# Kernel tuning notes

Hardware: AMD Instinct MI355X
Metric: run time of the kernel (lower is better)

The kernel has to match this reference:

```python
import jax, jax.numpy as jnp
import numpy as np

# real spherical-harmonics constants (3DGS convention)
C0 = 0.28209479177387814
C1 = 0.4886025119029199
C2 = (1.0925484305920792, -1.0925484305920792, 0.31539156525252005, -1.0925484305920792, 0.5462742152960396)
C3 = (-0.5900435899266435, 2.890611442640554, -0.4570457994644658, 0.3731763325901154, -0.4570457994644658, 1.445305721320277, -0.5900435899266435)


def eval_sh3(sh, dirs):
    # sh: [N,16,3], dirs: [N,3] unit view dirs -> [N,3]
    x, y, z = dirs[:, 0:1], dirs[:, 1:2], dirs[:, 2:3]
    xx, yy, zz = x * x, y * y, z * z
    xy, yz, xz = x * y, y * z, x * z
    res = C0 * sh[:, 0]
    res = res - C1 * y * sh[:, 1] + C1 * z * sh[:, 2] - C1 * x * sh[:, 3]
    res = (res + C2[0] * xy * sh[:, 4] + C2[1] * yz * sh[:, 5]
           + C2[2] * (2.0 * zz - xx - yy) * sh[:, 6]
           + C2[3] * xz * sh[:, 7] + C2[4] * (xx - yy) * sh[:, 8])
    res = (res + C3[0] * y * (3.0 * xx - yy) * sh[:, 9] + C3[1] * xy * z * sh[:, 10]
           + C3[2] * y * (4.0 * zz - xx - yy) * sh[:, 11]
           + C3[3] * z * (2.0 * zz - 3.0 * xx - 3.0 * yy) * sh[:, 12]
           + C3[4] * x * (4.0 * zz - xx - yy) * sh[:, 13]
           + C3[5] * z * (xx - yy) * sh[:, 14] + C3[6] * x * (xx - 3.0 * yy) * sh[:, 15])
    return res


def quat_to_rotmat(q):
    # q: [N,4] wxyz (normalized here)
    q = q / jnp.linalg.norm(q, axis=-1, keepdims=True)
    w, x, y, z = q[:, 0], q[:, 1], q[:, 2], q[:, 3]
    return jnp.stack([
        jnp.stack([1 - 2 * (y * y + z * z), 2 * (x * y - w * z), 2 * (x * z + w * y)], -1),
        jnp.stack([2 * (x * y + w * z), 1 - 2 * (x * x + z * z), 2 * (y * z - w * x)], -1),
        jnp.stack([2 * (x * z - w * y), 2 * (y * z + w * x), 1 - 2 * (x * x + y * y)], -1),
    ], -2)  # [N,3,3]


def setup_inputs() -> dict:
    key = jax.random.key(0)
    ks = jax.random.split(key, 6)
    N, K = 2048, 16
    means = jax.random.normal(ks[0], (N, 3), dtype=jnp.float32) * 1.5 + jnp.array([0.0, 0.0, 5.0])
    quats = jax.random.normal(ks[1], (N, 4), dtype=jnp.float32)
    scales = jax.random.normal(ks[2], (N, 3), dtype=jnp.float32) * 0.5 - 3.0  # log-scales (need_active)
    opacities = jax.random.normal(ks[3], (N,), dtype=jnp.float32)              # logits (need_active)
    colors = jax.random.normal(ks[4], (N, K, 3), dtype=jnp.float32) * 0.3
    camtoworlds = jnp.eye(4, dtype=jnp.float32)[None]                          # identity cam at origin
    W = H = 128
    f = 150.0
    Ks = jnp.array([[[f, 0.0, W / 2], [0.0, f, H / 2], [0.0, 0.0, 1.0]]], dtype=jnp.float32)
    return {"means": means, "quats": quats, "scales": scales, "opacities": opacities,
            "colors": colors, "camtoworlds": camtoworlds, "Ks": Ks, "width": W, "height": H}


def reference(means, quats, scales, opacities, colors, camtoworlds, Ks, width, height):
    # need_active=True path of GaussianSplattingRender.forward
    scales = jnp.exp(scales)
    opac = jax.nn.sigmoid(opacities)
    viewmat = jnp.linalg.inv(camtoworlds)[0]         # world->camera
    Rw, tw = viewmat[:3, :3], viewmat[:3, 3]
    t = means @ Rw.T + tw                            # [N,3] camera space
    depth = t[:, 2]
    tz = jnp.maximum(depth, 1e-2)
    K0 = Ks[0]
    fx, fy, cx, cy = K0[0, 0], K0[1, 1], K0[0, 2], K0[1, 2]
    u = fx * t[:, 0] / tz + cx                       # 2D means
    v = fy * t[:, 1] / tz + cy
    # 3D covariance = R S S^T R^T
    Rq = quat_to_rotmat(quats)                       # [N,3,3]
    M = Rq * scales[:, None, :]
    cov3d = M @ jnp.swapaxes(M, -1, -2)              # [N,3,3]
    covc = jnp.einsum('ij,njk,lk->nil', Rw, cov3d, Rw)
    # EWA projection Jacobian (pinhole)
    z1 = 1.0 / tz
    zeros = jnp.zeros_like(tz)
    J = jnp.stack([
        jnp.stack([fx * z1, zeros, -fx * t[:, 0] * z1 * z1], -1),
        jnp.stack([zeros, fy * z1, -fy * t[:, 1] * z1 * z1], -1),
    ], -2)                                           # [N,2,3]
    cov2d = jnp.einsum('nij,njk,nlk->nil', J, covc, J)
    a = cov2d[:, 0, 0] + 0.3                         # classic (non-antialiased) pixel blur
    c = cov2d[:, 1, 1] + 0.3
    b = cov2d[:, 0, 1]
    det = a * c - b * b
    ca, cb, cc = c / det, -b / det, a / det          # conic (inverse 2x2 cov)
    # SH -> RGB (sh_degree = sqrt(16)-1 = 3)
    campos = camtoworlds[0, :3, 3]
    dirs = means - campos
    dirs = dirs / jnp.linalg.norm(dirs, axis=-1, keepdims=True)
    rgb = jnp.maximum(eval_sh3(colors, dirs) + 0.5, 0.0)   # [N,3]
    # global front-to-back depth sort
    order = jnp.argsort(depth)
    us, vs = u[order], v[order]
    cas, cbs, ccs = ca[order], cb[order], cc[order]
    opac_s, rgb_s, depth_s = opac[order], rgb[order], depth[order]
    # pixel centers
    px = jnp.arange(width, dtype=jnp.float32) + 0.5
    py = jnp.arange(height, dtype=jnp.float32) + 0.5
    gx, gy = jnp.meshgrid(px, py)                    # [H,W]
    gx, gy = gx.reshape(-1), gy.reshape(-1)          # [P]
    dx = gx[None, :] - us[:, None]                   # [N,P]
    dy = gy[None, :] - vs[:, None]
    sigma = 0.5 * (cas[:, None] * dx * dx + ccs[:, None] * dy * dy) + cbs[:, None] * dx * dy
    alpha = opac_s[:, None] * jnp.exp(-jnp.maximum(sigma, 0.0))
    visible = (depth_s[:, None] > 1e-2) & (alpha >= 1.0 / 255.0)
    alpha = jnp.where(visible, jnp.minimum(alpha, 0.999), 0.0)
    # front-to-back alpha compositing: w_i = alpha_i * prod_{j<i}(1-alpha_j)
    T = jnp.cumprod(1.0 - alpha, axis=0)
    T_excl = jnp.concatenate([jnp.ones_like(T[:1]), T[:-1]], axis=0)
    w = alpha * T_excl                               # [N,P]
    render_colors = jnp.einsum('np,nc->pc', w, rgb_s).reshape(height, width, 3)[None]
    render_alphas = jnp.sum(w, axis=0).reshape(height, width, 1)[None]
    return render_colors, render_alphas
```

## Files before the change

kernel.cpp:

```cpp
#include <hip/hip_runtime.h>
#include <hip/hip_bf16.h>


__global__ void k_pre(const float* __restrict__ means, const float* __restrict__ quats,
                      const float* __restrict__ scales, const float* __restrict__ opacs,
                      const float* __restrict__ colors, const float* __restrict__ ct,
                      const float* __restrict__ Kmat, int N,
                      float* __restrict__ pre, int* __restrict__ rank) {
  int i = blockIdx.x * blockDim.x + threadIdx.x;
  if (i >= N) return;
  rank[i] = 0;

  float c00 = ct[0], c01 = ct[1], c02 = ct[2], c03 = ct[3];
  float c10 = ct[4], c11 = ct[5], c12 = ct[6], c13 = ct[7];
  float c20 = ct[8], c21 = ct[9], c22 = ct[10], c23 = ct[11];
  float W00 = c00, W01 = c10, W02 = c20;
  float W10 = c01, W11 = c11, W12 = c21;
  float W20 = c02, W21 = c12, W22 = c22;
  float tw0 = -(W00 * c03 + W01 * c13 + W02 * c23);
  float tw1 = -(W10 * c03 + W11 * c13 + W12 * c23);
  float tw2 = -(W20 * c03 + W21 * c13 + W22 * c23);
  float fx = Kmat[0], cx = Kmat[2], fy = Kmat[4], cy = Kmat[5];

  float mx = means[3 * i], my = means[3 * i + 1], mz = means[3 * i + 2];
  float tx = W00 * mx + W01 * my + W02 * mz + tw0;
  float ty = W10 * mx + W11 * my + W12 * mz + tw1;
  float depth = W20 * mx + W21 * my + W22 * mz + tw2;
  float tz = fmaxf(depth, 0.01f);
  float z1 = 1.0f / tz;
  float u = fx * tx * z1 + cx;
  float v = fy * ty * z1 + cy;

  float qw = quats[4 * i], qx = quats[4 * i + 1], qy = quats[4 * i + 2], qz = quats[4 * i + 3];
  float qn = rsqrtf(qw * qw + qx * qx + qy * qy + qz * qz);
  qw *= qn; qx *= qn; qy *= qn; qz *= qn;
  float sx = expf(scales[3 * i]), sy = expf(scales[3 * i + 1]), sz = expf(scales[3 * i + 2]);
  float r00 = 1.f - 2.f * (qy * qy + qz * qz);
  float r01 = 2.f * (qx * qy - qw * qz);
  float r02 = 2.f * (qx * qz + qw * qy);
  float r10 = 2.f * (qx * qy + qw * qz);
  float r11 = 1.f - 2.f * (qx * qx + qz * qz);
  float r12 = 2.f * (qy * qz - qw * qx);
  float r20 = 2.f * (qx * qz - qw * qy);
  float r21 = 2.f * (qy * qz + qw * qx);
  float r22 = 1.f - 2.f * (qx * qx + qy * qy);
  float m00 = r00 * sx, m01 = r01 * sy, m02 = r02 * sz;
  float m10 = r10 * sx, m11 = r11 * sy, m12 = r12 * sz;
  float m20 = r20 * sx, m21 = r21 * sy, m22 = r22 * sz;
  float S00 = m00 * m00 + m01 * m01 + m02 * m02;
  float S01 = m00 * m10 + m01 * m11 + m02 * m12;
  float S02 = m00 * m20 + m01 * m21 + m02 * m22;
  float S11 = m10 * m10 + m11 * m11 + m12 * m12;
  float S12 = m10 * m20 + m11 * m21 + m12 * m22;
  float S22 = m20 * m20 + m21 * m21 + m22 * m22;
  float A00 = W00 * S00 + W01 * S01 + W02 * S02;
  float A01 = W00 * S01 + W01 * S11 + W02 * S12;
  float A02 = W00 * S02 + W01 * S12 + W02 * S22;
  float A10 = W10 * S00 + W11 * S01 + W12 * S02;
  float A11 = W10 * S01 + W11 * S11 + W12 * S12;
  float A12 = W10 * S02 + W11 * S12 + W12 * S22;
  float A20 = W20 * S00 + W21 * S01 + W22 * S02;
  float A21 = W20 * S01 + W21 * S11 + W22 * S12;
  float A22 = W20 * S02 + W21 * S12 + W22 * S22;
  float V00 = A00 * W00 + A01 * W01 + A02 * W02;
  float V01 = A00 * W10 + A01 * W11 + A02 * W12;
  float V02 = A00 * W20 + A01 * W21 + A02 * W22;
  float V11 = A10 * W10 + A11 * W11 + A12 * W12;
  float V12 = A10 * W20 + A11 * W21 + A12 * W22;
  float V22 = A20 * W20 + A21 * W21 + A22 * W22;
  float j00 = fx * z1, j02 = -fx * tx * z1 * z1;
  float j11 = fy * z1, j12 = -fy * ty * z1 * z1;
  float g2_00 = j00 * j00 * V00 + 2.f * j00 * j02 * V02 + j02 * j02 * V22;
  float g2_01 = j00 * j11 * V01 + j00 * j12 * V02 + j02 * j11 * V12 + j02 * j12 * V22;
  float g2_11 = j11 * j11 * V11 + 2.f * j11 * j12 * V12 + j12 * j12 * V22;
  float a2 = g2_00 + 0.3f;
  float cc2 = g2_11 + 0.3f;
  float b2 = g2_01;
  float det = a2 * cc2 - b2 * b2;
  float idet = 1.0f / det;
  float conA = cc2 * idet, conB = -b2 * idet, conC = a2 * idet;

  float op = 1.0f / (1.0f + __expf(-opacs[i]));
  if (!(depth > 0.01f)) op = 0.0f;

  float lt = logf(255.f * op);
  float lam = 0.5f * (a2 + cc2) +
              sqrtf(0.25f * (a2 - cc2) * (a2 - cc2) + b2 * b2);
  float rad = (lt > 0.f) ? (sqrtf(2.02f * lam * lt) + 1.0f) : 0.f;

  float dxm = mx - c03, dym = my - c13, dzm = mz - c23;
  float dn = rsqrtf(dxm * dxm + dym * dym + dzm * dzm);
  float x = dxm * dn, y = dym * dn, z = dzm * dn;
  float xx = x * x, yy = y * y, zz = z * z;
  float xy = x * y, yz = y * z, xz = x * z;
  float k[16];
  k[0] = 0.28209479177387814f;
  k[1] = -0.4886025119029199f * y;
  k[2] = 0.4886025119029199f * z;
  k[3] = -0.4886025119029199f * x;
  k[4] = 1.0925484305920792f * xy;
  k[5] = -1.0925484305920792f * yz;
  k[6] = 0.31539156525252005f * (2.f * zz - xx - yy);
  k[7] = -1.0925484305920792f * xz;
  k[8] = 0.5462742152960396f * (xx - yy);
  k[9]  = -0.5900435899266435f * y * (3.f * xx - yy);
  k[10] = 2.890611442640554f * xy * z;
  k[11] = -0.4570457994644658f * y * (4.f * zz - xx - yy);
  k[12] = 0.3731763325901154f * z * (2.f * zz - 3.f * xx - 3.f * yy);
  k[13] = -0.4570457994644658f * x * (4.f * zz - xx - yy);
  k[14] = 1.445305721320277f * z * (xx - yy);
  k[15] = -0.5900435899266435f * x * (xx - 3.f * yy);
  float rr = 0.f, gg = 0.f, bb = 0.f;
  const float* col = colors + (size_t)i * 48;
#pragma unroll
  for (int j = 0; j < 16; ++j) {
    rr += k[j] * col[3 * j];
    gg += k[j] * col[3 * j + 1];
    bb += k[j] * col[3 * j + 2];
  }
  rr = fmaxf(rr + 0.5f, 0.f);
  gg = fmaxf(gg + 0.5f, 0.f);
  bb = fmaxf(bb + 0.5f, 0.f);

  pre[0 * N + i] = depth;
  pre[1 * N + i] = u;
  pre[2 * N + i] = v;
  pre[3 * N + i] = 0.5f * conA;
  pre[4 * N + i] = conB;
  pre[5 * N + i] = 0.5f * conC;
  pre[6 * N + i] = op;
  pre[7 * N + i] = rr;
  pre[8 * N + i] = gg;
  pre[9 * N + i] = bb;
  pre[10 * N + i] = rad;
}

__global__ void k_rank(const float* __restrict__ pre, int N, int* __restrict__ rank) {
  __shared__ float sd[256];
  int i = blockIdx.x * 256 + threadIdx.x;
  float di = (i < N) ? pre[i] : 0.f;
  int chunk = (N + 7) >> 3;
  int jbase = blockIdx.y * chunk;
  int jend = min(N, jbase + chunk);
  int cnt = 0;
  for (int c0 = jbase; c0 < jend; c0 += 256) {
    int j = c0 + threadIdx.x;
    sd[threadIdx.x] = (j < jend) ? pre[j] : 0.f;
    __syncthreads();
    int lim = min(256, jend - c0);
    for (int jj = 0; jj < lim; ++jj) {
      float dj = sd[jj];
      int gj = c0 + jj;
      cnt += (dj < di || (dj == di && gj < i)) ? 1 : 0;
    }
    __syncthreads();
  }
  if (i < N && cnt > 0) atomicAdd(&rank[i], cnt);
}

__global__ void k_scatter(const float* __restrict__ pre, int N, const int* __restrict__ rank,
                          float* __restrict__ srt, float4* __restrict__ bbox) {
  int i = blockIdx.x * 256 + threadIdx.x;
  if (i >= N) return;
  int r = rank[i];
  float* dst = srt + (size_t)r * 12;
#pragma unroll
  for (int f = 0; f < 9; ++f) dst[f] = pre[(f + 1) * N + i];
  float u = pre[1 * N + i], v = pre[2 * N + i], rad = pre[10 * N + i];
  bbox[r] = make_float4(u - rad, v - rad, u + rad, v + rad);
}

__global__ __launch_bounds__(512) void k_render(const float* __restrict__ srt,
                                                const float4* __restrict__ bbox, int N,
                                                float* __restrict__ out, int Wimg,
                                                int tilesX, int P) {
  __shared__ int lst[2048];
  __shared__ float red[8][5][64];
  __shared__ int wcnt[8];

  int t = threadIdx.x;
  int lane = t & 63;
  int w = __builtin_amdgcn_readfirstlane(t >> 6);
  int tile = blockIdx.x;
  int tx = tile % tilesX, ty = tile / tilesX;
  float x0 = tx * 8 + 0.5f, x1 = tx * 8 + 7.5f;
  float y0 = ty * 8 + 0.5f, y1 = ty * 8 + 7.5f;

  int base = 0;
  for (int c0 = 0; c0 < N; c0 += 512) {
    int g = c0 + t;
    bool keep = false;
    if (g < N) {
      float4 bb = bbox[g];
      keep = (bb.x <= x1) & (bb.z >= x0) & (bb.y <= y1) & (bb.w >= y0);
    }
    unsigned long long m = __ballot(keep);
    if (lane == 0) wcnt[w] = __popcll(m);
    __syncthreads();
    int woff = base;
    for (int k = 0; k < w; ++k) woff += wcnt[k];
    int tot = 0;
#pragma unroll
    for (int k = 0; k < 8; ++k) tot += wcnt[k];
    if (keep) lst[woff + __popcll(m & ((1ull << lane) - 1ull))] = g;
    base += tot;
    __syncthreads();
  }
  int cnt = base;

  float gx = tx * 8 + (lane & 7) + 0.5f;
  float gy = ty * 8 + (lane >> 3) + 0.5f;
  int chunk = (cnt + 7) >> 3;
  int g0 = w * chunk;
  int g1 = min(cnt, g0 + chunk);

  const float4* s4 = (const float4*)srt;
  float T = 1.0f, accr = 0.f, accg = 0.f, accb = 0.f, acca = 0.f;
  for (int g = g0; g < g1; ++g) {
    int idx = lst[g];
    float4 a = s4[idx * 3 + 0];
    float4 b = s4[idx * 3 + 1];
    float4 c = s4[idx * 3 + 2];
    float dx = gx - a.x, dy = gy - a.y;
    float s = a.z * dx * dx + b.x * dy * dy + a.w * dx * dy;
    float e = __expf(-fmaxf(s, 0.f));
    float al = b.y * e;
    al = (al >= 0.00392156862745098f) ? fminf(al, 0.999f) : 0.f;
    float wgt = al * T;
    accr = fmaf(wgt, b.z, accr);
    accg = fmaf(wgt, b.w, accg);
    accb = fmaf(wgt, c.x, accb);
    acca += wgt;
    T *= 1.f - al;
  }
  red[w][0][lane] = accr;
  red[w][1][lane] = accg;
  red[w][2][lane] = accb;
  red[w][3][lane] = acca;
  red[w][4][lane] = T;
  __syncthreads();

  if (t < 64) {
    float Tr = 1.f, R = 0.f, G = 0.f, B = 0.f, A = 0.f;
#pragma unroll
    for (int k = 0; k < 8; ++k) {
      R += Tr * red[k][0][t];
      G += Tr * red[k][1][t];
      B += Tr * red[k][2][t];
      A += Tr * red[k][3][t];
      Tr *= red[k][4][t];
    }
    int pix = (ty * 8 + (t >> 3)) * Wimg + tx * 8 + (t & 7);
    out[pix * 3 + 0] = R;
    out[pix * 3 + 1] = G;
    out[pix * 3 + 2] = B;
    out[(size_t)P * 3 + pix] = A;
  }
}

extern "C" void kernel_launch(void* const* d_in, const int* in_sizes, int n_in,
                              void* d_out, int out_size, void* d_ws, size_t ws_size,
                              hipStream_t stream) {
  const float* means  = (const float*)d_in[0];
  const float* quats  = (const float*)d_in[1];
  const float* scales = (const float*)d_in[2];
  const float* opacs  = (const float*)d_in[3];
  const float* colors = (const float*)d_in[4];
  const float* ct     = (const float*)d_in[5];
  const float* Kmat   = (const float*)d_in[6];
  const int*   pW     = (const int*)d_in[7];
  const int*   pH     = (const int*)d_in[8];
  (void)pW; (void)pH;

  int N = in_sizes[0] / 3;
  int P = out_size / 4;
  int Wimg = 128;
  int Himg = P / Wimg;
  int tilesX = Wimg / 8, tilesY = Himg / 8;

  float*  pre  = (float*)d_ws;
  float*  srt  = pre + (size_t)11 * N;
  float4* bbox = (float4*)(srt + (size_t)12 * N);
  int*    rank = (int*)(bbox + N);

  int nb = (N + 255) / 256;
  k_pre<<<nb, 256, 0, stream>>>(means, quats, scales, opacs, colors, ct, Kmat, N, pre, rank);
  dim3 rg(nb, 8);
  k_rank<<<rg, 256, 0, stream>>>(pre, N, rank);
  k_scatter<<<nb, 256, 0, stream>>>(pre, N, rank, srt, bbox);
  k_render<<<tilesX * tilesY, 512, 0, stream>>>(srt, bbox, N, (float*)d_out, Wimg, tilesX, P);
}
```

Baseline: 89.81 us.

## Fuse depth-rank counting and scatter into one kernel without atomics

Merges the rank and scatter kernels so each thread counts the full depth comparison itself and then writes its sorted record directly. This removes the rank buffer, its zeroing, the atomic adds and one kernel launch. In exchange the rank grid shrinks from 64 blocks to 8 blocks, each looping over all N, so there is much less parallelism for the O(N^2) comparison.

```diff
diff --git a/kernel.cpp b/kernel.cpp
--- a/kernel.cpp
+++ b/kernel.cpp
@@ -6,10 +6,9 @@
                       const float* __restrict__ scales, const float* __restrict__ opacs,
                       const float* __restrict__ colors, const float* __restrict__ ct,
                       const float* __restrict__ Kmat, int N,
-                      float* __restrict__ pre, int* __restrict__ rank) {
+                      float* __restrict__ pre) {
   int i = blockIdx.x * blockDim.x + threadIdx.x;
   if (i >= N) return;
-  rank[i] = 0;
 
   float c00 = ct[0], c01 = ct[1], c02 = ct[2], c03 = ct[3];
   float c10 = ct[4], c11 = ct[5], c12 = ct[6], c13 = ct[7];
@@ -135,19 +134,17 @@
   pre[10 * N + i] = rad;
 }
 
-__global__ void k_rank(const float* __restrict__ pre, int N, int* __restrict__ rank) {
+__global__ void k_ranksc(const float* __restrict__ pre, int N,
+                         float* __restrict__ srt, float4* __restrict__ bbox) {
   __shared__ float sd[256];
   int i = blockIdx.x * 256 + threadIdx.x;
   float di = (i < N) ? pre[i] : 0.f;
-  int chunk = (N + 7) >> 3;
-  int jbase = blockIdx.y * chunk;
-  int jend = min(N, jbase + chunk);
   int cnt = 0;
-  for (int c0 = jbase; c0 < jend; c0 += 256) {
+  for (int c0 = 0; c0 < N; c0 += 256) {
     int j = c0 + threadIdx.x;
-    sd[threadIdx.x] = (j < jend) ? pre[j] : 0.f;
-    __syncthreads();
-    int lim = min(256, jend - c0);
+    sd[threadIdx.x] = (j < N) ? pre[j] : 0.f;
+    __syncthreads();
+    int lim = min(256, N - c0);
     for (int jj = 0; jj < lim; ++jj) {
       float dj = sd[jj];
       int gj = c0 + jj;
@@ -155,19 +152,12 @@
     }
     __syncthreads();
   }
-  if (i < N && cnt > 0) atomicAdd(&rank[i], cnt);
-}
-
-__global__ void k_scatter(const float* __restrict__ pre, int N, const int* __restrict__ rank,
-                          float* __restrict__ srt, float4* __restrict__ bbox) {
-  int i = blockIdx.x * 256 + threadIdx.x;
   if (i >= N) return;
-  int r = rank[i];
-  float* dst = srt + (size_t)r * 12;
+  float* dst = srt + (size_t)cnt * 12;
 #pragma unroll
   for (int f = 0; f < 9; ++f) dst[f] = pre[(f + 1) * N + i];
   float u = pre[1 * N + i], v = pre[2 * N + i], rad = pre[10 * N + i];
-  bbox[r] = make_float4(u - rad, v - rad, u + rad, v + rad);
+  bbox[cnt] = make_float4(u - rad, v - rad, u + rad, v + rad);
 }
 
 __global__ __launch_bounds__(512) void k_render(const float* __restrict__ srt,
@@ -268,9 +258,6 @@
   const float* colors = (const float*)d_in[4];
   const float* ct     = (const float*)d_in[5];
   const float* Kmat   = (const float*)d_in[6];
-  const int*   pW     = (const int*)d_in[7];
-  const int*   pH     = (const int*)d_in[8];
-  (void)pW; (void)pH;
 
   int N = in_sizes[0] / 3;
   int P = out_size / 4;
@@ -281,12 +268,9 @@
   float*  pre  = (float*)d_ws;
   float*  srt  = pre + (size_t)11 * N;
   float4* bbox = (float4*)(srt + (size_t)12 * N);
-  int*    rank = (int*)(bbox + N);
 
   int nb = (N + 255) / 256;
-  k_pre<<<nb, 256, 0, stream>>>(means, quats, scales, opacs, colors, ct, Kmat, N, pre, rank);
-  dim3 rg(nb, 8);
-  k_rank<<<rg, 256, 0, stream>>>(pre, N, rank);
-  k_scatter<<<nb, 256, 0, stream>>>(pre, N, rank, srt, bbox);
+  k_pre<<<nb, 256, 0, stream>>>(means, quats, scales, opacs, colors, ct, Kmat, N, pre);
+  k_ranksc<<<nb, 256, 0, stream>>>(pre, N, srt, bbox);
   k_render<<<tilesX * tilesY, 512, 0, stream>>>(srt, bbox, N, (float*)d_out, Wimg, tilesX, P);
 }
```

After: 137.9 us. 1.54x slower.
